# Optimization experiments

Hardware: AMD Instinct MI355X
Metric: run time of the kernel (lower is better)

## Reference

```python
import jax, jax.numpy as jnp
import numpy as np

NUM_EXPERTS = 8
GROUP_SIZE = 2
NUM_GROUPS = NUM_EXPERTS // GROUP_SIZE
NUM_SLOTS = 128
HIDDEN = 2048
D_FF = int(HIDDEN * 4 * (2.0 / 3.0))  # 5461
BATCH = 4
SEQ = 2048
BS = BATCH * SEQ


def setup_inputs() -> dict:
    key = jax.random.key(0)
    k0, k1, k2, k3 = jax.random.split(key, 4)
    x = jax.random.normal(k0, (BS, HIDDEN), dtype=jnp.float32)
    router_weights = jax.random.normal(k1, (BS, NUM_EXPERTS), dtype=jnp.float32)
    up_w = jax.random.normal(k2, (NUM_GROUPS, HIDDEN, D_FF), dtype=jnp.float32) * np.float32(1.0 / np.sqrt(HIDDEN))
    up_b = jnp.zeros((NUM_GROUPS, D_FF), dtype=jnp.float32)
    down_w = jax.random.normal(k3, (NUM_EXPERTS, D_FF, HIDDEN), dtype=jnp.float32) * np.float32(1.0 / np.sqrt(D_FF))
    down_b = jnp.zeros((NUM_EXPERTS, HIDDEN), dtype=jnp.float32)
    return {
        "x": x,
        "router_weights": router_weights,
        "up_w": up_w,
        "up_b": up_b,
        "down_w": down_w,
        "down_b": down_b,
        "batch_size": BATCH,
        "seq_len": SEQ,
    }


def reference(x, router_weights, up_w, up_b, down_w, down_b, batch_size, seq_len):
    # --- soft routing matrices (Soft-MoE; source raises NotImplementedError) ---
    h = router_weights                                   # (bs, E) routing logits
    dispatch = jax.nn.softmax(h, axis=0)                 # normalize over tokens per expert
    P = jnp.broadcast_to(dispatch[:, None, :], (h.shape[0], NUM_SLOTS, NUM_EXPERTS))  # (bs, k, E)
    G = jnp.full((NUM_SLOTS, NUM_EXPERTS), 1.0 / NUM_SLOTS, dtype=x.dtype)            # expert-choice combine (k, E)

    # --- dispatch: expert slot inputs ---
    tokens_for_expert = jnp.einsum('bke,bh->ekh', P, x)  # (E, k, hidden)

    # --- per-expert FFN (grouped up proj shared within each expert group) ---
    group_idx = np.arange(NUM_EXPERTS) // GROUP_SIZE     # static gather of shared up weights
    up_w_e = up_w[group_idx]                             # (E, hidden, d_ff)
    up_b_e = up_b[group_idx]                             # (E, d_ff)
    mid = jax.nn.silu(jnp.einsum('ekh,ehf->ekf', tokens_for_expert, up_w_e) + up_b_e[:, None, :])
    E_out = jnp.einsum('ekf,efh->ekh', mid, down_w) + down_b[:, None, :]  # (E, k, hidden)

    # --- combine (expert-choice branch): 'bs k e, k e, e k h -> bs h' ---
    y = jnp.einsum('bke,ke,ekh->bh', P, G, E_out)
    return y.reshape(batch_size, seq_len, HIDDEN)
```

## Files before the change

kernel.cpp:

```cpp
#include <hip/hip_runtime.h>

typedef float f4 __attribute__((ext_vector_type(4)));

#define HID 2048
#define DFF 5461
#define NE  8

#define WS_M  0
#define WS_IS 8
#define WS_T  64
#define WS_EO 16448

#define SC_TP 0
#define SC_MP 2097152
#define SC_EP 2796288

__device__ __forceinline__ void merge_ms(float& m, float& s, float mo, float so) {
  float mn = fmaxf(m, mo);
  s = s * __expf(m - mn) + so * __expf(mo - mn);
  m = mn;
}

__global__ __launch_bounds__(256) void k_stats(const float* __restrict__ rw,
                                               float* __restrict__ ws) {
  int e = blockIdx.x, tid = threadIdx.x;
  float m = -3.0e38f, s = 0.f;
#pragma unroll 4
  for (int r = 0; r < 32; r++) {
    float v = rw[(size_t)(r * 256 + tid) * NE + e];
    float mn = fmaxf(m, v);
    s = s * __expf(m - mn) + __expf(v - mn);
    m = mn;
  }
#pragma unroll
  for (int off = 32; off >= 1; off >>= 1) {
    float mo = __shfl_xor(m, off, 64);
    float so = __shfl_xor(s, off, 64);
    merge_ms(m, s, mo, so);
  }
  __shared__ float ml[4], sl[4];
  if ((tid & 63) == 0) { ml[tid >> 6] = m; sl[tid >> 6] = s; }
  __syncthreads();
  if (tid == 0) {
#pragma unroll
    for (int w = 1; w < 4; w++) merge_ms(m, s, ml[w], sl[w]);
    ws[WS_M + e] = m;
    ws[WS_IS + e] = 1.f / s;
  }
}

__global__ __launch_bounds__(256) void k_tpart(const float* __restrict__ x,
                                               const float* __restrict__ rw,
                                               const float* __restrict__ ws,
                                               float* __restrict__ sc) {
  __shared__ f4 dv4[64][2];
  __shared__ f4 red[3][NE][64];
  int tid = threadIdx.x;
  int rc = blockIdx.y, b0 = rc * 64;
  if (tid < 128) {
    int row = tid >> 1, half = tid & 1;
    const float* rp = rw + (size_t)(b0 + row) * NE + half * 4;
    int e0 = half * 4;
    f4 d;
    d.x = __expf(rp[0] - ws[WS_M + e0 + 0]) * ws[WS_IS + e0 + 0];
    d.y = __expf(rp[1] - ws[WS_M + e0 + 1]) * ws[WS_IS + e0 + 1];
    d.z = __expf(rp[2] - ws[WS_M + e0 + 2]) * ws[WS_IS + e0 + 2];
    d.w = __expf(rp[3] - ws[WS_M + e0 + 3]) * ws[WS_IS + e0 + 3];
    dv4[row][half] = d;
  }
  __syncthreads();
  int col = tid & 63, rg = tid >> 6;
  int c4 = blockIdx.x * 64 + col;
  f4 acc[NE];
#pragma unroll
  for (int e = 0; e < NE; e++) acc[e] = (f4){0.f, 0.f, 0.f, 0.f};
  const f4* x4 = (const f4*)x;
#pragma unroll 4
  for (int r = 0; r < 16; r++) {
    int row = rg * 16 + r;
    f4 xv = __builtin_nontemporal_load(&x4[(size_t)(b0 + row) * 512 + c4]);
    f4 dlo = dv4[row][0], dhi = dv4[row][1];
    acc[0] += dlo.x * xv;
    acc[1] += dlo.y * xv;
    acc[2] += dlo.z * xv;
    acc[3] += dlo.w * xv;
    acc[4] += dhi.x * xv;
    acc[5] += dhi.y * xv;
    acc[6] += dhi.z * xv;
    acc[7] += dhi.w * xv;
  }
  if (rg) {
#pragma unroll
    for (int e = 0; e < NE; e++) red[rg - 1][e][col] = acc[e];
  }
  __syncthreads();
  if (!rg) {
    f4* o4 = (f4*)(sc + SC_TP);
#pragma unroll
    for (int e = 0; e < NE; e++) {
      f4 a = acc[e] + red[0][e][col] + red[1][e][col] + red[2][e][col];
      o4[(size_t)(rc * NE + e) * 512 + c4] = a;
    }
  }
}

__global__ __launch_bounds__(256) void k_tred(const float* __restrict__ sc,
                                              float* __restrict__ ws) {
  __shared__ float red[8][32];
  int tid = threadIdx.x;
  int o = tid & 31, grp = tid >> 5;
  int i = blockIdx.x * 32 + o;
  double a = 0.0;
#pragma unroll 4
  for (int k = 0; k < 16; k++)
    a += (double)sc[SC_TP + (size_t)(grp * 16 + k) * (NE * HID) + i];
  red[grp][o] = (float)a;
  __syncthreads();
  if (tid < 32) {
    int ii = blockIdx.x * 32 + tid;
    float s = 0.f;
#pragma unroll
    for (int g = 0; g < 8; g++) s += red[g][tid];
    ws[WS_T + ii] = s;
  }
}

__global__ __launch_bounds__(256) void k_midpart(const float* __restrict__ up_w,
                                                 const float* __restrict__ ws,
                                                 float* __restrict__ sc) {
  int fb = blockIdx.x, hc = blockIdx.y, g = blockIdx.z;
  int tid = threadIdx.x;
  __shared__ float t0[128], t1[128];
  int h0 = hc * 128;
  if (tid < 128) t0[tid] = ws[WS_T + (2 * g) * HID + h0 + tid];
  else t1[tid - 128] = ws[WS_T + (2 * g + 1) * HID + h0 + tid - 128];
  __syncthreads();
  int fA = fb * 512 + tid;
  int fB = fA + 256;
  bool hasB = fB < DFF;
  const float* wp = up_w + ((size_t)g * HID + h0) * DFF;
  float a0 = 0.f, a1 = 0.f, bb0 = 0.f, bb1 = 0.f;
#pragma unroll 8
  for (int h = 0; h < 128; h++) {
    float wA = __builtin_nontemporal_load(wp + (size_t)h * DFF + fA);
    float wB = hasB ? __builtin_nontemporal_load(wp + (size_t)h * DFF + fB) : 0.f;
    a0 += t0[h] * wA;
    a1 += t1[h] * wA;
    bb0 += t0[h] * wB;
    bb1 += t1[h] * wB;
  }
  float* mp = sc + SC_MP + (size_t)hc * NE * DFF;
  mp[(size_t)(2 * g) * DFF + fA] = a0;
  mp[(size_t)(2 * g + 1) * DFF + fA] = a1;
  if (hasB) {
    mp[(size_t)(2 * g) * DFF + fB] = bb0;
    mp[(size_t)(2 * g + 1) * DFF + fB] = bb1;
  }
}

__global__ __launch_bounds__(256) void k_eopart(const float* __restrict__ down_w,
                                                const float* __restrict__ up_b,
                                                const float* __restrict__ sc_mp,
                                                float* __restrict__ sc) {
  int hb = blockIdx.x, fc = blockIdx.y, e = blockIdx.z;
  int tid = threadIdx.x;
  int f0 = fc * 43;
  const f4* base4 = (const f4*)down_w + ((size_t)e * DFF + f0) * 512 + hb * 256 + tid;
  f4 w[8];
#pragma unroll
  for (int j = 0; j < 8; j++)
    w[j] = __builtin_nontemporal_load(&base4[(size_t)j * 512]);
  __shared__ float ml[4][43];
  int lane = tid & 63, wv = tid >> 6;
  if (lane < 43) {
    double a = (double)up_b[(size_t)(e >> 1) * DFF + f0 + lane];
#pragma unroll 4
    for (int k = 0; k < 16; k++)
      a += (double)sc_mp[SC_MP + (size_t)(k * NE + e) * DFF + f0 + lane];
    float af = (float)a;
    ml[wv][lane] = af / (1.f + __expf(-af));
  }
  f4 acc = (f4){0.f, 0.f, 0.f, 0.f};
  for (int blk = 0; blk < 5; blk++) {
#pragma unroll
    for (int j = 0; j < 8; j++) {
      int cur = blk * 8 + j;
      f4 c = w[j];
      int nxt = cur + 8;
      if (nxt < 43) w[j] = __builtin_nontemporal_load(&base4[(size_t)nxt * 512]);
      acc += ml[wv][cur] * c;
    }
  }
#pragma unroll
  for (int j = 0; j < 3; j++) acc += ml[wv][40 + j] * w[j];
  ((f4*)(sc + SC_EP))[(size_t)(fc * NE + e) * 512 + hb * 256 + tid] = acc;
}

__global__ __launch_bounds__(256) void k_eored(const float* __restrict__ sc,
                                               const float* __restrict__ down_b,
                                               float* __restrict__ ws) {
  __shared__ float red[8][32];
  int tid = threadIdx.x;
  int o = tid & 31, grp = tid >> 5;
  int i = blockIdx.x * 32 + o;
  double a = 0.0;
  for (int fc = grp; fc < 127; fc += 8)
    a += (double)sc[SC_EP + (size_t)fc * (NE * HID) + i];
  red[grp][o] = (float)a;
  __syncthreads();
  if (tid < 32) {
    int ii = blockIdx.x * 32 + tid;
    float s = down_b[ii];
#pragma unroll
    for (int g = 0; g < 8; g++) s += red[g][tid];
    ws[WS_EO + ii] = s;
  }
}

__global__ __launch_bounds__(256) void k_comb(const float* __restrict__ rw,
                                              const float* __restrict__ ws,
                                              float* __restrict__ y) {
  int tid = threadIdx.x;
  int b0 = blockIdx.x * 16;
  __shared__ float dvl[16][NE];
  if (tid < 128) {
    int tok = tid >> 3, e = tid & 7;
    dvl[tok][e] = __expf(rw[(size_t)(b0 + tok) * NE + e] - ws[WS_M + e]) *
                  ws[WS_IS + e];
  }
  __syncthreads();
  const f4* eo4 = (const f4*)(ws + WS_EO);
  f4 ea[NE], eb[NE];
#pragma unroll
  for (int e = 0; e < NE; e++) {
    ea[e] = eo4[e * 512 + tid];
    eb[e] = eo4[e * 512 + 256 + tid];
  }
  f4* y4 = (f4*)y;
#pragma unroll 4
  for (int t = 0; t < 16; t++) {
    f4 o0 = (f4){0.f, 0.f, 0.f, 0.f};
    f4 o1 = (f4){0.f, 0.f, 0.f, 0.f};
#pragma unroll
    for (int e = 0; e < NE; e++) {
      float d = dvl[t][e];
      o0 += d * ea[e];
      o1 += d * eb[e];
    }
    __builtin_nontemporal_store(o0, &y4[(size_t)(b0 + t) * 512 + tid]);
    __builtin_nontemporal_store(o1, &y4[(size_t)(b0 + t) * 512 + 256 + tid]);
  }
}

extern "C" void kernel_launch(void* const* d_in, const int* in_sizes, int n_in,
                              void* d_out, int out_size, void* d_ws, size_t ws_size,
                              hipStream_t stream) {
  const float* x      = (const float*)d_in[0];
  const float* rw     = (const float*)d_in[1];
  const float* up_w   = (const float*)d_in[2];
  const float* up_b   = (const float*)d_in[3];
  const float* down_w = (const float*)d_in[4];
  const float* down_b = (const float*)d_in[5];
  float* y  = (float*)d_out;
  float* ws = (float*)d_ws;
  float* sc = y;

  hipLaunchKernelGGL(k_stats, dim3(8), dim3(256), 0, stream, rw, ws);
  hipLaunchKernelGGL(k_tpart, dim3(8, 128), dim3(256), 0, stream, x, rw, ws, sc);
  hipLaunchKernelGGL(k_tred, dim3(512), dim3(256), 0, stream, sc, ws);
  hipLaunchKernelGGL(k_midpart, dim3(11, 16, 4), dim3(256), 0, stream, up_w, ws, sc);
  hipLaunchKernelGGL(k_eopart, dim3(2, 127, 8), dim3(256), 0, stream, down_w, up_b, sc, sc);
  hipLaunchKernelGGL(k_eored, dim3(512), dim3(256), 0, stream, sc, down_b, ws);
  hipLaunchKernelGGL(k_comb, dim3(512), dim3(256), 0, stream, rw, ws, y);
}
```

Baseline: 137.9 us.

## Fold softmax statistics into token-partial kernel and defer normalization

```diff
diff --git a/kernel.cpp b/kernel.cpp
--- a/kernel.cpp
+++ b/kernel.cpp
@@ -6,89 +6,63 @@
 #define DFF 5461
 #define NE  8
 
-#define WS_M  0
-#define WS_IS 8
+#define WS_IS 0
 #define WS_T  64
 #define WS_EO 16448
 
 #define SC_TP 0
-#define SC_MP 2097152
-#define SC_EP 2796288
-
-__device__ __forceinline__ void merge_ms(float& m, float& s, float mo, float so) {
-  float mn = fmaxf(m, mo);
-  s = s * __expf(m - mn) + so * __expf(mo - mn);
-  m = mn;
-}
-
-__global__ __launch_bounds__(256) void k_stats(const float* __restrict__ rw,
-                                               float* __restrict__ ws) {
-  int e = blockIdx.x, tid = threadIdx.x;
-  float m = -3.0e38f, s = 0.f;
-#pragma unroll 4
-  for (int r = 0; r < 32; r++) {
-    float v = rw[(size_t)(r * 256 + tid) * NE + e];
-    float mn = fmaxf(m, v);
-    s = s * __expf(m - mn) + __expf(v - mn);
-    m = mn;
-  }
-#pragma unroll
-  for (int off = 32; off >= 1; off >>= 1) {
-    float mo = __shfl_xor(m, off, 64);
-    float so = __shfl_xor(s, off, 64);
-    merge_ms(m, s, mo, so);
-  }
-  __shared__ float ml[4], sl[4];
-  if ((tid & 63) == 0) { ml[tid >> 6] = m; sl[tid >> 6] = s; }
-  __syncthreads();
-  if (tid == 0) {
-#pragma unroll
-    for (int w = 1; w < 4; w++) merge_ms(m, s, ml[w], sl[w]);
-    ws[WS_M + e] = m;
-    ws[WS_IS + e] = 1.f / s;
-  }
-}
+#define SC_TS 1048576
+#define SC_MP 1049600
+#define SC_EP 1748736
 
 __global__ __launch_bounds__(256) void k_tpart(const float* __restrict__ x,
                                                const float* __restrict__ rw,
-                                               const float* __restrict__ ws,
                                                float* __restrict__ sc) {
   __shared__ f4 dv4[64][2];
   __shared__ f4 red[3][NE][64];
   int tid = threadIdx.x;
-  int rc = blockIdx.y, b0 = rc * 64;
-  if (tid < 128) {
-    int row = tid >> 1, half = tid & 1;
-    const float* rp = rw + (size_t)(b0 + row) * NE + half * 4;
-    int e0 = half * 4;
-    f4 d;
-    d.x = __expf(rp[0] - ws[WS_M + e0 + 0]) * ws[WS_IS + e0 + 0];
-    d.y = __expf(rp[1] - ws[WS_M + e0 + 1]) * ws[WS_IS + e0 + 1];
-    d.z = __expf(rp[2] - ws[WS_M + e0 + 2]) * ws[WS_IS + e0 + 2];
-    d.w = __expf(rp[3] - ws[WS_M + e0 + 3]) * ws[WS_IS + e0 + 3];
-    dv4[row][half] = d;
-  }
-  __syncthreads();
+  int rc = blockIdx.y;
   int col = tid & 63, rg = tid >> 6;
   int c4 = blockIdx.x * 64 + col;
+  const f4* x4 = (const f4*)x;
   f4 acc[NE];
 #pragma unroll
   for (int e = 0; e < NE; e++) acc[e] = (f4){0.f, 0.f, 0.f, 0.f};
-  const f4* x4 = (const f4*)x;
-#pragma unroll 4
-  for (int r = 0; r < 16; r++) {
-    int row = rg * 16 + r;
-    f4 xv = __builtin_nontemporal_load(&x4[(size_t)(b0 + row) * 512 + c4]);
-    f4 dlo = dv4[row][0], dhi = dv4[row][1];
-    acc[0] += dlo.x * xv;
-    acc[1] += dlo.y * xv;
-    acc[2] += dlo.z * xv;
-    acc[3] += dlo.w * xv;
-    acc[4] += dhi.x * xv;
-    acc[5] += dhi.y * xv;
-    acc[6] += dhi.z * xv;
-    acc[7] += dhi.w * xv;
-  }
+  double spart = 0.0;
+  for (int sub = 0; sub < 2; sub++) {
+    int b0 = rc * 128 + sub * 64;
+    if (tid < 128) {
+      int row = tid >> 1, half = tid & 1;
+      const float* rp = rw + (size_t)(b0 + row) * NE + half * 4;
+      f4 d;
+      d.x = __expf(rp[0]);
+      d.y = __expf(rp[1]);
+      d.z = __expf(rp[2]);
+      d.w = __expf(rp[3]);
+      dv4[row][half] = d;
+    }
+    __syncthreads();
+    if (blockIdx.x == 0 && tid < NE) {
+      const float* dp = (const float*)dv4;
+      for (int row = 0; row < 64; row++) spart += (double)dp[row * 8 + tid];
+    }
+#pragma unroll 4
+    for (int r = 0; r < 16; r++) {
+      int row = rg * 16 + r;
+      f4 xv = __builtin_nontemporal_load(&x4[(size_t)(b0 + row) * 512 + c4]);
+      f4 dlo = dv4[row][0], dhi = dv4[row][1];
+      acc[0] += dlo.x * xv;
+      acc[1] += dlo.y * xv;
+      acc[2] += dlo.z * xv;
+      acc[3] += dlo.w * xv;
+      acc[4] += dhi.x * xv;
+      acc[5] += dhi.y * xv;
+      acc[6] += dhi.z * xv;
+      acc[7] += dhi.w * xv;
+    }
+    __syncthreads();
+  }
+  if (blockIdx.x == 0 && tid < NE) sc[SC_TS + rc * NE + tid] = (float)spart;
   if (rg) {
 #pragma unroll
     for (int e = 0; e < NE; e++) red[rg - 1][e][col] = acc[e];
@@ -107,13 +81,21 @@
 __global__ __launch_bounds__(256) void k_tred(const float* __restrict__ sc,
                                               float* __restrict__ ws) {
   __shared__ float red[8][32];
-  int tid = threadIdx.x;
+  __shared__ float sinv[NE];
+  int tid = threadIdx.x;
+  if (tid < NE) {
+    double s = 0.0;
+    for (int ch = 0; ch < 64; ch++) s += (double)sc[SC_TS + ch * NE + tid];
+    float inv = (float)(1.0 / s);
+    sinv[tid] = inv;
+    if (blockIdx.x == 0) ws[WS_IS + tid] = inv;
+  }
   int o = tid & 31, grp = tid >> 5;
   int i = blockIdx.x * 32 + o;
   double a = 0.0;
 #pragma unroll 4
-  for (int k = 0; k < 16; k++)
-    a += (double)sc[SC_TP + (size_t)(grp * 16 + k) * (NE * HID) + i];
+  for (int k = 0; k < 8; k++)
+    a += (double)sc[SC_TP + (size_t)(grp * 8 + k) * (NE * HID) + i];
   red[grp][o] = (float)a;
   __syncthreads();
   if (tid < 32) {
@@ -121,7 +103,7 @@
     float s = 0.f;
 #pragma unroll
     for (int g = 0; g < 8; g++) s += red[g][tid];
-    ws[WS_T + ii] = s;
+    ws[WS_T + ii] = s * sinv[ii >> 11];
   }
 }
 
@@ -225,8 +207,7 @@
   __shared__ float dvl[16][NE];
   if (tid < 128) {
     int tok = tid >> 3, e = tid & 7;
-    dvl[tok][e] = __expf(rw[(size_t)(b0 + tok) * NE + e] - ws[WS_M + e]) *
-                  ws[WS_IS + e];
+    dvl[tok][e] = __expf(rw[(size_t)(b0 + tok) * NE + e]) * ws[WS_IS + e];
   }
   __syncthreads();
   const f4* eo4 = (const f4*)(ws + WS_EO);
@@ -265,8 +246,7 @@
   float* ws = (float*)d_ws;
   float* sc = y;
 
-  hipLaunchKernelGGL(k_stats, dim3(8), dim3(256), 0, stream, rw, ws);
-  hipLaunchKernelGGL(k_tpart, dim3(8, 128), dim3(256), 0, stream, x, rw, ws, sc);
+  hipLaunchKernelGGL(k_tpart, dim3(8, 64), dim3(256), 0, stream, x, rw, sc);
   hipLaunchKernelGGL(k_tred, dim3(512), dim3(256), 0, stream, sc, ws);
   hipLaunchKernelGGL(k_midpart, dim3(11, 16, 4), dim3(256), 0, stream, up_w, ws, sc);
   hipLaunchKernelGGL(k_eopart, dim3(2, 127, 8), dim3(256), 0, stream, down_w, up_b, sc, sc);
```

Result: faster. 132.1 us (-4.2%).
